# Kernel tuning notes

Measured on AMD Instinct MI355X. Metric: run time of the kernel, lower is better.

## Reference

```python
import jax, jax.numpy as jnp
import numpy as np

N_NODES = 100000
N_EDGES = 1600000
IN_FEAT = 256
OUT_FEAT = 64


def setup_inputs() -> dict:
    key = jax.random.key(0)
    k1, k2, k3, k4, k5 = jax.random.split(key, 5)
    feat = jax.random.normal(k1, (N_NODES, IN_FEAT), dtype=jnp.float32)
    # Xavier-uniform-like init for the weight
    limit = float(np.sqrt(6.0 / (IN_FEAT + OUT_FEAT)))
    weight = jax.random.uniform(k2, (IN_FEAT, OUT_FEAT), dtype=jnp.float32,
                                minval=-limit, maxval=limit)
    # Sparse adjacency in COO form: rows sorted for segment_sum efficiency
    adj_rows = jnp.sort(jax.random.randint(k3, (N_EDGES,), 0, N_NODES, dtype=jnp.int64))
    adj_cols = jax.random.randint(k4, (N_EDGES,), 0, N_NODES, dtype=jnp.int64)
    adj_vals = jax.random.uniform(k5, (N_EDGES,), dtype=jnp.float32)
    return {"feat": feat, "weight": weight, "adj_rows": adj_rows,
            "adj_cols": adj_cols, "adj_vals": adj_vals}


def reference(feat, weight, adj_rows, adj_cols, adj_vals):
    # out = adj @ (feat @ W), adj sparse COO -> gather + weighted scatter-add
    proj = feat @ weight                       # [N, out_feat] dense mm
    msgs = adj_vals[:, None] * proj[adj_cols]  # [E, out_feat] gather
    out = jax.ops.segment_sum(msgs, adj_rows, num_segments=feat.shape[0],
                              indices_are_sorted=True)
    return out
```

## Files before the change

kernel.cpp:

```cpp
#include <hip/hip_runtime.h>
#include <cstdint>

#define IN_FEAT 256
#define OUT_FEAT 64

constexpr int EPW = 64;

typedef __attribute__((ext_vector_type(4))) float f32x4;
typedef __attribute__((ext_vector_type(8))) __bf16 bf16x8;

union BF8 { unsigned short u[8]; bf16x8 v; };

__device__ inline unsigned short f2bf(float f) {
    unsigned u = __builtin_bit_cast(unsigned, f);
    unsigned r = u + 0x7fffu + ((u >> 16) & 1u);
    return (unsigned short)(r >> 16);
}
__device__ inline float bf2f(unsigned short h) {
    return __builtin_bit_cast(float, (unsigned)h << 16);
}

__global__ __launch_bounds__(256) void gemm_proj_mfma(
    const float* __restrict__ feat, const float* __restrict__ W,
    unsigned short* __restrict__ projb, int n_rows)
{
    __shared__ unsigned short sWb[8 * 4 * 64 * 8];

    {
        const int c   = threadIdx.x & 63;
        const int kg0 = threadIdx.x >> 6;
        #pragma unroll
        for (int it = 0; it < 8; ++it) {
            const int kg = it * 4 + kg0;
            BF8 tmp;
            #pragma unroll
            for (int j = 0; j < 8; ++j)
                tmp.u[j] = f2bf(W[(kg * 8 + j) * OUT_FEAT + c]);
            const int ks = kg >> 2;
            const int l  = (kg & 3) * 16 + (c & 15);
            const int ct = c >> 4;
            *reinterpret_cast<bf16x8*>(&sWb[((ks * 4 + ct) * 64 + l) * 8]) = tmp.v;
        }
    }
    __syncthreads();

    const int lane = threadIdx.x & 63;
    const int wave = threadIdx.x >> 6;
    const int row0 = blockIdx.x * 64 + wave * 16;
    if (row0 >= n_rows) return;

    const int kgrp = lane >> 4;
    int ar = row0 + (lane & 15);
    if (ar >= n_rows) ar = n_rows - 1;

    f32x4 fa[16];
    const float* fp = feat + (size_t)ar * IN_FEAT + kgrp * 8;
    #pragma unroll
    for (int ks = 0; ks < 8; ++ks) {
        fa[2 * ks]     = *reinterpret_cast<const f32x4*>(fp + ks * 32);
        fa[2 * ks + 1] = *reinterpret_cast<const f32x4*>(fp + ks * 32 + 4);
    }

    f32x4 acc[4];
    #pragma unroll
    for (int ct = 0; ct < 4; ++ct) acc[ct] = f32x4{0.f, 0.f, 0.f, 0.f};

    #pragma unroll
    for (int ks = 0; ks < 8; ++ks) {
        BF8 Ah, Al;
        #pragma unroll
        for (int h = 0; h < 2; ++h) {
            const f32x4 v = fa[2 * ks + h];
            #pragma unroll
            for (int j = 0; j < 4; ++j) {
                const float f = v[j];
                const unsigned short hb = f2bf(f);
                Ah.u[h * 4 + j] = hb;
                Al.u[h * 4 + j] = f2bf(f - bf2f(hb));
            }
        }
        #pragma unroll
        for (int ct = 0; ct < 4; ++ct) {
            BF8 B;
            B.v = *reinterpret_cast<const bf16x8*>(
                &sWb[((ks * 4 + ct) * 64 + lane) * 8]);
            acc[ct] = __builtin_amdgcn_mfma_f32_16x16x32_bf16(Ah.v, B.v, acc[ct], 0, 0, 0);
            acc[ct] = __builtin_amdgcn_mfma_f32_16x16x32_bf16(Al.v, B.v, acc[ct], 0, 0, 0);
        }
    }

    #pragma unroll
    for (int r = 0; r < 4; ++r) {
        const int row = row0 + kgrp * 4 + r;
        if (row < n_rows) {
            #pragma unroll
            for (int ct = 0; ct < 4; ++ct)
                projb[(size_t)row * OUT_FEAT + ct * 16 + (lane & 15)] =
                    f2bf(acc[ct][r]);
        }
    }
}

__global__ __launch_bounds__(256) void gather_scatter(
    const unsigned short* __restrict__ projb, const int* __restrict__ rows,
    const int* __restrict__ cols, const float* __restrict__ vals,
    float* __restrict__ out, int n_edges)
{
    const int lane = threadIdx.x & 63;
    const long wid = (long)((blockIdx.x * 256 + threadIdx.x) >> 6);
    const long e0 = wid * EPW;
    if (e0 >= n_edges) return;

    const long ee = (e0 + lane < n_edges) ? (e0 + lane) : (n_edges - 1);
    const int r_v = rows[ee];
    const int c_v = cols[ee];
    const int v_bits = (e0 + lane < n_edges)
                         ? __builtin_bit_cast(int, vals[ee]) : 0;

    unsigned short p[EPW];
    #pragma unroll
    for (int i = 0; i < EPW; ++i) {
        const int c = __builtin_amdgcn_readlane(c_v, i);
        p[i] = projb[(size_t)c * OUT_FEAT + lane];
    }

    float acc = 0.f;
    int cur = __builtin_amdgcn_readlane(r_v, 0);
    #pragma unroll
    for (int i = 0; i < EPW; ++i) {
        const int   r = __builtin_amdgcn_readlane(r_v, i);
        const float v = __builtin_bit_cast(float, __builtin_amdgcn_readlane(v_bits, i));
        if (r != cur) {
            atomicAdd(out + (size_t)cur * OUT_FEAT + lane, acc);
            acc = 0.f;
            cur = r;
        }
        acc = fmaf(v, bf2f(p[i]), acc);
    }
    atomicAdd(out + (size_t)cur * OUT_FEAT + lane, acc);
}

extern "C" void kernel_launch(void* const* d_in, const int* in_sizes, int n_in,
                              void* d_out, int out_size, void* d_ws, size_t ws_size,
                              hipStream_t stream)
{
    const float* feat     = (const float*)d_in[0];
    const float* weight   = (const float*)d_in[1];
    const int*   adj_rows = (const int*)d_in[2];
    const int*   adj_cols = (const int*)d_in[3];
    const float* adj_vals = (const float*)d_in[4];
    float*       out      = (float*)d_out;
    unsigned short* projb = (unsigned short*)d_ws;

    const int n_nodes = in_sizes[0] / IN_FEAT;
    const int n_edges = in_sizes[2];

    hipMemsetAsync(d_out, 0, (size_t)out_size * sizeof(float), stream);

    const int gemm_blocks = (n_nodes + 63) / 64;
    gemm_proj_mfma<<<gemm_blocks, 256, 0, stream>>>(feat, weight, projb, n_nodes);

    const int waves  = (n_edges + EPW - 1) / EPW;
    const int blocks = (waves + 3) / 4;
    gather_scatter<<<blocks, 256, 0, stream>>>(projb, adj_rows, adj_cols,
                                               adj_vals, out, n_edges);
}
```

Baseline: 67.30 us.

## Switch projection to fp16 MFMA and use plain stores for interior segments

Replaces the split-bf16 (hi+lo) two-MFMA projection with a single fp16 conversion and one fp16 MFMA per tile, halving the matrix work and dropping the residual conversion math. The global feat loads are issued before the shared-memory weight staging so the two overlap. In the scatter, segments that are neither first nor last in a wave's edge window are written with plain stores instead of atomics, since sorted rows mean only the boundary segments can be shared with another wave. fp16 has less range and a different rounding than split bf16, which could change accuracy.

```diff
diff --git a/kernel.cpp b/kernel.cpp
--- a/kernel.cpp
+++ b/kernel.cpp
@@ -7,48 +7,19 @@
 constexpr int EPW = 64;
 
 typedef __attribute__((ext_vector_type(4))) float f32x4;
-typedef __attribute__((ext_vector_type(8))) __bf16 bf16x8;
+typedef __attribute__((ext_vector_type(8))) _Float16 f16x8;
 
-union BF8 { unsigned short u[8]; bf16x8 v; };
-
-__device__ inline unsigned short f2bf(float f) {
-    unsigned u = __builtin_bit_cast(unsigned, f);
-    unsigned r = u + 0x7fffu + ((u >> 16) & 1u);
-    return (unsigned short)(r >> 16);
-}
-__device__ inline float bf2f(unsigned short h) {
-    return __builtin_bit_cast(float, (unsigned)h << 16);
-}
+union HF8 { _Float16 h[8]; f16x8 v; };
 
 __global__ __launch_bounds__(256) void gemm_proj_mfma(
     const float* __restrict__ feat, const float* __restrict__ W,
-    unsigned short* __restrict__ projb, int n_rows)
+    _Float16* __restrict__ projh, int n_rows)
 {
-    __shared__ unsigned short sWb[8 * 4 * 64 * 8];
-
-    {
-        const int c   = threadIdx.x & 63;
-        const int kg0 = threadIdx.x >> 6;
-        #pragma unroll
-        for (int it = 0; it < 8; ++it) {
-            const int kg = it * 4 + kg0;
-            BF8 tmp;
-            #pragma unroll
-            for (int j = 0; j < 8; ++j)
-                tmp.u[j] = f2bf(W[(kg * 8 + j) * OUT_FEAT + c]);
-            const int ks = kg >> 2;
-            const int l  = (kg & 3) * 16 + (c & 15);
-            const int ct = c >> 4;
-            *reinterpret_cast<bf16x8*>(&sWb[((ks * 4 + ct) * 64 + l) * 8]) = tmp.v;
-        }
-    }
-    __syncthreads();
+    __shared__ _Float16 sWh[8 * 4 * 64 * 8];
 
     const int lane = threadIdx.x & 63;
     const int wave = threadIdx.x >> 6;
     const int row0 = blockIdx.x * 64 + wave * 16;
-    if (row0 >= n_rows) return;
-
     const int kgrp = lane >> 4;
     int ar = row0 + (lane & 15);
     if (ar >= n_rows) ar = n_rows - 1;
@@ -61,31 +32,45 @@
         fa[2 * ks + 1] = *reinterpret_cast<const f32x4*>(fp + ks * 32 + 4);
     }
 
+    {
+        const int c   = threadIdx.x & 63;
+        const int kg0 = threadIdx.x >> 6;
+        #pragma unroll
+        for (int it = 0; it < 8; ++it) {
+            const int kg = it * 4 + kg0;
+            HF8 tmp;
+            #pragma unroll
+            for (int j = 0; j < 8; ++j)
+                tmp.h[j] = (_Float16)W[(kg * 8 + j) * OUT_FEAT + c];
+            const int ks = kg >> 2;
+            const int l  = (kg & 3) * 16 + (c & 15);
+            const int ct = c >> 4;
+            *reinterpret_cast<f16x8*>(&sWh[((ks * 4 + ct) * 64 + l) * 8]) = tmp.v;
+        }
+    }
+    __syncthreads();
+    if (row0 >= n_rows) return;
+
     f32x4 acc[4];
     #pragma unroll
     for (int ct = 0; ct < 4; ++ct) acc[ct] = f32x4{0.f, 0.f, 0.f, 0.f};
 
     #pragma unroll
     for (int ks = 0; ks < 8; ++ks) {
-        BF8 Ah, Al;
+        HF8 A;
         #pragma unroll
         for (int h = 0; h < 2; ++h) {
             const f32x4 v = fa[2 * ks + h];
             #pragma unroll
-            for (int j = 0; j < 4; ++j) {
-                const float f = v[j];
-                const unsigned short hb = f2bf(f);
-                Ah.u[h * 4 + j] = hb;
-                Al.u[h * 4 + j] = f2bf(f - bf2f(hb));
-            }
+            for (int j = 0; j < 4; ++j)
+                A.h[h * 4 + j] = (_Float16)v[j];
         }
         #pragma unroll
         for (int ct = 0; ct < 4; ++ct) {
-            BF8 B;
-            B.v = *reinterpret_cast<const bf16x8*>(
-                &sWb[((ks * 4 + ct) * 64 + lane) * 8]);
-            acc[ct] = __builtin_amdgcn_mfma_f32_16x16x32_bf16(Ah.v, B.v, acc[ct], 0, 0, 0);
-            acc[ct] = __builtin_amdgcn_mfma_f32_16x16x32_bf16(Al.v, B.v, acc[ct], 0, 0, 0);
+            HF8 B;
+            B.v = *reinterpret_cast<const f16x8*>(
+                &sWh[((ks * 4 + ct) * 64 + lane) * 8]);
+            acc[ct] = __builtin_amdgcn_mfma_f32_16x16x32_f16(A.v, B.v, acc[ct], 0, 0, 0);
         }
     }
 
@@ -95,14 +80,14 @@
         if (row < n_rows) {
             #pragma unroll
             for (int ct = 0; ct < 4; ++ct)
-                projb[(size_t)row * OUT_FEAT + ct * 16 + (lane & 15)] =
-                    f2bf(acc[ct][r]);
+                projh[(size_t)row * OUT_FEAT + ct * 16 + (lane & 15)] =
+                    (_Float16)acc[ct][r];
         }
     }
 }
 
 __global__ __launch_bounds__(256) void gather_scatter(
-    const unsigned short* __restrict__ projb, const int* __restrict__ rows,
+    const _Float16* __restrict__ projh, const int* __restrict__ rows,
     const int* __restrict__ cols, const float* __restrict__ vals,
     float* __restrict__ out, int n_edges)
 {
@@ -117,25 +102,29 @@
     const int v_bits = (e0 + lane < n_edges)
                          ? __builtin_bit_cast(int, vals[ee]) : 0;
 
-    unsigned short p[EPW];
+    _Float16 p[EPW];
     #pragma unroll
     for (int i = 0; i < EPW; ++i) {
         const int c = __builtin_amdgcn_readlane(c_v, i);
-        p[i] = projb[(size_t)c * OUT_FEAT + lane];
+        p[i] = projh[(size_t)c * OUT_FEAT + lane];
     }
 
     float acc = 0.f;
     int cur = __builtin_amdgcn_readlane(r_v, 0);
+    bool first_seg = true;
     #pragma unroll
     for (int i = 0; i < EPW; ++i) {
         const int   r = __builtin_amdgcn_readlane(r_v, i);
         const float v = __builtin_bit_cast(float, __builtin_amdgcn_readlane(v_bits, i));
         if (r != cur) {
-            atomicAdd(out + (size_t)cur * OUT_FEAT + lane, acc);
+            float* dst = out + (size_t)cur * OUT_FEAT + lane;
+            if (first_seg) atomicAdd(dst, acc);
+            else           *dst = acc;
+            first_seg = false;
             acc = 0.f;
             cur = r;
         }
-        acc = fmaf(v, bf2f(p[i]), acc);
+        acc = fmaf(v, (float)p[i], acc);
     }
     atomicAdd(out + (size_t)cur * OUT_FEAT + lane, acc);
 }
@@ -150,7 +139,7 @@
     const int*   adj_cols = (const int*)d_in[3];
     const float* adj_vals = (const float*)d_in[4];
     float*       out      = (float*)d_out;
-    unsigned short* projb = (unsigned short*)d_ws;
+    _Float16*    projh    = (_Float16*)d_ws;
 
     const int n_nodes = in_sizes[0] / IN_FEAT;
     const int n_edges = in_sizes[2];
@@ -158,10 +147,10 @@
     hipMemsetAsync(d_out, 0, (size_t)out_size * sizeof(float), stream);
 
     const int gemm_blocks = (n_nodes + 63) / 64;
-    gemm_proj_mfma<<<gemm_blocks, 256, 0, stream>>>(feat, weight, projb, n_nodes);
+    gemm_proj_mfma<<<gemm_blocks, 256, 0, stream>>>(feat, weight, projh, n_nodes);
 
     const int waves  = (n_edges + EPW - 1) / EPW;
     const int blocks = (waves + 3) / 4;
-    gather_scatter<<<blocks, 256, 0, stream>>>(projb, adj_rows, adj_cols,
+    gather_scatter<<<blocks, 256, 0, stream>>>(projh, adj_rows, adj_cols,
                                                adj_vals, out, n_edges);
 }
```

Measured after the change: 65.00 us. 1.04x faster.
